# Kernel optimization log

Hardware: AMD Instinct MI355X
Metric: run time of the kernel (lower is better)

Reference implementation:

```python
import jax, jax.numpy as jnp
import numpy as np

B, S, D, H, HD, L, P = 32, 511, 512, 8, 64, 4, 501
PD = 32
FD = D - 2 * PD  # feature_proj output dim = hidden - 2*player_dim
DFF = 4 * D


def _pe(T, d):
    pos = jnp.arange(T, dtype=jnp.float32)[:, None]
    div = jnp.exp(jnp.arange(0, d, 2, dtype=jnp.float32) * (-np.log(10000.0) / d))
    pe = jnp.zeros((T, d), jnp.float32)
    pe = pe.at[:, 0::2].set(jnp.sin(pos * div))
    pe = pe.at[:, 1::2].set(jnp.cos(pos * div))
    return pe


def _ln(x, g, b, eps=1e-5):
    mu = x.mean(-1, keepdims=True)
    v = jnp.mean((x - mu) ** 2, -1, keepdims=True)
    return (x - mu) * jax.lax.rsqrt(v + eps) * g + b


def _forward(runs, wickets, overs, batters, bowlers, player_embed, Wf, bf,
             query_token, Wq, bq, Wk, bk, Wv, bv, Wo, bo,
             rec_s, bow_s, bat_s, W1, b1, W2, b2, g1, be1, g2, be2, Wout, bout):
    Bt, St = runs.shape
    T = St + 1
    # ball embedding: [B,S,3]@[3,FD] cat player embeds -> [B,S,D]
    feats = jnp.stack([runs, wickets, overs], -1) @ Wf + bf
    x = jnp.concatenate([feats, player_embed[batters], player_embed[bowlers]], -1)
    # append learned query token, add sinusoidal PE
    x = jnp.concatenate([x, jnp.broadcast_to(query_token, (Bt, 1, D))], 1)
    x = x + _pe(T, D)[None]
    # actor masks, padded with ones for the query row/col -> [B,T,T]
    sb = (bowlers[:, :, None] == bowlers[:, None, :]).astype(x.dtype)
    sm = (batters[:, :, None] == batters[:, None, :]).astype(x.dtype)
    row = jnp.ones((Bt, 1, St), x.dtype)
    col = jnp.ones((Bt, T, 1), x.dtype)
    sb = jnp.concatenate([jnp.concatenate([sb, row], 1), col], 2)
    sm = jnp.concatenate([jnp.concatenate([sm, row], 1), col], 2)
    causal = jnp.triu(jnp.ones((T, T), bool), 1)
    rec = jnp.arange(T, dtype=x.dtype) / T  # recency bias over key positions
    scale = 1.0 / np.float32(np.sqrt(HD))
    for l in range(L):
        q = (x @ Wq[l] + bq[l]).reshape(Bt, T, H, HD).transpose(0, 2, 1, 3)
        k = (x @ Wk[l] + bk[l]).reshape(Bt, T, H, HD).transpose(0, 2, 1, 3)
        v = (x @ Wv[l] + bv[l]).reshape(Bt, T, H, HD).transpose(0, 2, 1, 3)
        scores = jnp.einsum('bhqd,bhkd->bhqk', q, k) * scale
        # specialized head biases (num_heads >= 3)
        scores = scores.at[:, 0].add((rec_s[l] * rec)[None, None, :])
        scores = scores.at[:, 1].add(bow_s[l] * sb)
        scores = scores.at[:, 2].add(bat_s[l] * sm)
        scores = jnp.where(causal[None, None], -jnp.inf, scores)
        a = jax.nn.softmax(scores, axis=-1)
        o = jnp.einsum('bhqk,bhkd->bhqd', a, v).transpose(0, 2, 1, 3).reshape(Bt, T, D)
        x = _ln(x + o @ Wo[l] + bo[l], g1[l], be1[l])
        ff = jax.nn.gelu(x @ W1[l] + b1[l], approximate=False) @ W2[l] + b2[l]
        x = _ln(x + ff, g2[l], be2[l])
    return x[:, -1] @ Wout + bout  # [B, D]


def setup_inputs() -> dict:
    key = jax.random.key(0)
    ks = jax.random.split(key, 16)
    w = lambda k, sh: (0.02 * jax.random.normal(k, sh)).astype(jnp.float32)
    return {
        'runs': jax.random.uniform(ks[0], (B, S), jnp.float32),
        'wickets': jax.random.uniform(ks[1], (B, S), jnp.float32),
        'overs': jax.random.uniform(ks[2], (B, S), jnp.float32),
        'batters': jax.random.randint(ks[3], (B, S), 0, 500, jnp.int32),
        'bowlers': jax.random.randint(ks[4], (B, S), 0, 500, jnp.int32),
        'player_embed': w(ks[5], (P, PD)),
        'Wf': w(ks[6], (3, FD)), 'bf': jnp.zeros((FD,), jnp.float32),
        'query_token': jax.random.normal(ks[7], (1, 1, D), jnp.float32),
        'Wq': w(ks[8], (L, D, D)), 'bq': jnp.zeros((L, D), jnp.float32),
        'Wk': w(ks[9], (L, D, D)), 'bk': jnp.zeros((L, D), jnp.float32),
        'Wv': w(ks[10], (L, D, D)), 'bv': jnp.zeros((L, D), jnp.float32),
        'Wo': w(ks[11], (L, D, D)), 'bo': jnp.zeros((L, D), jnp.float32),
        'rec_s': jnp.full((L,), 0.5, jnp.float32),
        'bow_s': jnp.full((L,), 2.0, jnp.float32),
        'bat_s': jnp.full((L,), 2.0, jnp.float32),
        'W1': w(ks[12], (L, D, DFF)), 'b1': jnp.zeros((L, DFF), jnp.float32),
        'W2': w(ks[13], (L, DFF, D)), 'b2': jnp.zeros((L, D), jnp.float32),
        'g1': jnp.ones((L, D), jnp.float32), 'be1': jnp.zeros((L, D), jnp.float32),
        'g2': jnp.ones((L, D), jnp.float32), 'be2': jnp.zeros((L, D), jnp.float32),
        'Wout': w(ks[14], (D, D)), 'bout': jnp.zeros((D,), jnp.float32),
    }


def reference(runs, wickets, overs, batters, bowlers, player_embed, Wf, bf,
              query_token, Wq, bq, Wk, bk, Wv, bv, Wo, bo,
              rec_s, bow_s, bat_s, W1, b1, W2, b2, g1, be1, g2, be2, Wout, bout):
    return _forward(runs, wickets, overs, batters, bowlers, player_embed, Wf, bf,
                    query_token, Wq, bq, Wk, bk, Wv, bv, Wo, bo,
                    rec_s, bow_s, bat_s, W1, b1, W2, b2, g1, be1, g2, be2, Wout, bout)
```

## Files before the change

kernel.cpp:

```cpp
#include <hip/hip_runtime.h>
#include <math.h>

#define B_ 32
#define S_ 511
#define T_ 512
#define D_ 512
#define H_ 8
#define HD_ 64
#define L_ 4
#define P_ 501
#define PD_ 32
#define FD_ 448
#define DFF_ 2048

typedef __attribute__((ext_vector_type(8))) short bf16x8;
typedef __attribute__((ext_vector_type(4))) float f32x4;

__device__ __forceinline__ unsigned short f2bf(float f) {
  union { float f; unsigned int u; } c; c.f = f;
  unsigned int r = c.u + 0x7FFFu + ((c.u >> 16) & 1u);
  return (unsigned short)(r >> 16);
}

__global__ __launch_bounds__(256) void wtrans_kernel(
    const float* __restrict__ in, unsigned short* __restrict__ out, int K, int N)
{
  __shared__ float t[64][65];
  const int l = blockIdx.z;
  in  += (size_t)l * K * N;
  out += (size_t)l * N * K;
  const int k0 = blockIdx.x * 64, n0 = blockIdx.y * 64;
  const int tx = threadIdx.x & 63, ty = threadIdx.x >> 6;
#pragma unroll
  for (int i = 0; i < 16; ++i) {
    int r = ty + i * 4;
    t[r][tx] = in[(size_t)(k0 + r) * N + n0 + tx];
  }
  __syncthreads();
#pragma unroll
  for (int i = 0; i < 16; ++i) {
    int r = ty + i * 4;
    out[(size_t)(n0 + r) * K + k0 + tx] = f2bf(t[tx][r]);
  }
}

__global__ __launch_bounds__(256) void embed_kernel(
    const float* __restrict__ runs, const float* __restrict__ wickets,
    const float* __restrict__ overs, const int* __restrict__ batters,
    const int* __restrict__ bowlers, const float* __restrict__ pemb,
    const float* __restrict__ Wf, const float* __restrict__ bfv,
    const float* __restrict__ qtok, float* __restrict__ x,
    unsigned short* __restrict__ xb)
{
  size_t idx = (size_t)blockIdx.x * 256 + threadIdx.x;
  const size_t total = (size_t)B_ * T_ * D_;
  if (idx >= total) return;
  int d = (int)(idx % D_);
  int t = (int)((idx / D_) % T_);
  int b = (int)(idx / ((size_t)D_ * T_));
  float val;
  if (t < S_) {
    size_t st = (size_t)b * S_ + t;
    if (d < FD_) {
      val = runs[st] * Wf[d] + wickets[st] * Wf[FD_ + d] + overs[st] * Wf[2 * FD_ + d] + bfv[d];
    } else if (d < FD_ + PD_) {
      val = pemb[(size_t)batters[st] * PD_ + (d - FD_)];
    } else {
      val = pemb[(size_t)bowlers[st] * PD_ + (d - FD_ - PD_)];
    }
  } else {
    val = qtok[d];
  }
  float div = expf((float)(2 * (d >> 1)) * (-9.210340371976184f / (float)D_));
  float ang = (float)t * div;
  val += (d & 1) ? cosf(ang) : sinf(ang);
  x[idx] = val;
  xb[idx] = f2bf(val);
}

template<int ACT>
__global__ __launch_bounds__(256) void mfma_gemm(
    const unsigned short* __restrict__ A, const unsigned short* __restrict__ Bt,
    const float* __restrict__ bias, float* __restrict__ C,
    unsigned short* __restrict__ Cb, int N, int K)
{
  __shared__ unsigned short As[128 * 32];
  __shared__ unsigned short Bs[128 * 32];
  const int tid = threadIdx.x;
  const int m0 = blockIdx.y * 128, n0 = blockIdx.x * 128;
  const int lane = tid & 63, w = tid >> 6;
  const int wr = w >> 1, wc = w & 1;
  const int lr = lane & 15, lg = lane >> 4;

  f32x4 acc[4][4] = {};

  const int sr = tid >> 2, sc8 = (tid & 3) * 8;
  const unsigned short* gA = A + (size_t)(m0 + sr) * K + sc8;
  const unsigned short* gB = Bt + (size_t)(n0 + sr) * K + sc8;
  const size_t rowK64 = (size_t)64 * K;

  for (int k0 = 0; k0 < K; k0 += 32) {
    __syncthreads();
    *(bf16x8*)&As[sr * 32 + sc8]        = *(const bf16x8*)(gA + k0);
    *(bf16x8*)&As[(sr + 64) * 32 + sc8] = *(const bf16x8*)(gA + rowK64 + k0);
    *(bf16x8*)&Bs[sr * 32 + sc8]        = *(const bf16x8*)(gB + k0);
    *(bf16x8*)&Bs[(sr + 64) * 32 + sc8] = *(const bf16x8*)(gB + rowK64 + k0);
    __syncthreads();
    bf16x8 af[4], bfr[4];
#pragma unroll
    for (int f = 0; f < 4; ++f) {
      af[f]  = *(const bf16x8*)&As[(wr * 64 + f * 16 + lr) * 32 + lg * 8];
      bfr[f] = *(const bf16x8*)&Bs[(wc * 64 + f * 16 + lr) * 32 + lg * 8];
    }
#pragma unroll
    for (int i = 0; i < 4; ++i)
#pragma unroll
      for (int j = 0; j < 4; ++j)
        acc[i][j] = __builtin_amdgcn_mfma_f32_16x16x32_bf16(af[i], bfr[j], acc[i][j], 0, 0, 0);
  }

  const int crow0 = m0 + wr * 64 + lg * 4;
  const int ccol0 = n0 + wc * 64 + lr;
#pragma unroll
  for (int i = 0; i < 4; ++i) {
#pragma unroll
    for (int j = 0; j < 4; ++j) {
      const int col = ccol0 + j * 16;
      const float bcol = bias[col];
#pragma unroll
      for (int r = 0; r < 4; ++r) {
        const int row = crow0 + i * 16 + r;
        float v = acc[i][j][r] + bcol;
        if (ACT == 1) {
          v = 0.5f * v * (1.0f + erff(v * 0.70710678118654752f));
          Cb[(size_t)row * N + col] = f2bf(v);
        } else if (ACT == 2) {
          Cb[(size_t)row * N + col] = f2bf(v);
        } else {
          C[(size_t)row * N + col] = v;
        }
      }
    }
  }
}

__global__ __launch_bounds__(256) void vtrans_kernel(
    const unsigned short* __restrict__ vb, unsigned short* __restrict__ vt)
{
  __shared__ unsigned short tile[64 * 65];
  const int t0 = blockIdx.x * 64, h = blockIdx.y, b = blockIdx.z;
  const int tid = threadIdx.x;
  const int r = tid >> 2, ch = (tid & 3) * 16;
  const unsigned short* src = vb + ((size_t)b * T_ + t0 + r) * D_ + h * HD_ + ch;
  *(bf16x8*)&tile[r * 65 + ch]     = *(const bf16x8*)src;
  *(bf16x8*)&tile[r * 65 + ch + 8] = *(const bf16x8*)(src + 8);
  __syncthreads();
  unsigned short tmp[16];
#pragma unroll
  for (int j = 0; j < 16; ++j) tmp[j] = tile[(ch + j) * 65 + r];
  unsigned short* dst = vt + ((size_t)(b * H_ + h) * HD_ + r) * T_ + t0 + ch;
  *(bf16x8*)dst       = *(const bf16x8*)&tmp[0];
  *(bf16x8*)(dst + 8) = *(const bf16x8*)&tmp[8];
}

__global__ __launch_bounds__(256) void flash_mfma_kernel(
    const unsigned short* __restrict__ q, const unsigned short* __restrict__ k,
    const unsigned short* __restrict__ vt, unsigned short* __restrict__ o,
    const int* __restrict__ batters, const int* __restrict__ bowlers,
    const float* __restrict__ rec_sp, const float* __restrict__ bow_sp,
    const float* __restrict__ bat_sp, int l)
{
  __shared__ unsigned short QPs[64 * 70];
  __shared__ unsigned short Ks[64 * 70];
  __shared__ unsigned short Vs[64 * 70];
  __shared__ int aq_s[64], ak_s[64];

  const int qt = blockIdx.x, h = blockIdx.y, b = blockIdx.z;
  const int tid = threadIdx.x;
  const int w = tid >> 6, lane = tid & 63;
  const int c = lane & 15, g = lane >> 4;
  const int q0 = qt * 64;

  int mode = 0; float hs = 0.f;
  if (h == 0) { mode = 1; hs = rec_sp[l]; }
  else if (h == 1) { mode = 2; hs = bow_sp[l]; }
  else if (h == 2) { mode = 3; hs = bat_sp[l]; }
  const int* actors = (mode == 2) ? bowlers : batters;

  {
    const int r = tid >> 2, ch = (tid & 3) * 16;
    const unsigned short* src = q + ((size_t)b * T_ + q0 + r) * D_ + h * HD_ + ch;
    *(bf16x8*)&QPs[r * 70 + ch]     = *(const bf16x8*)src;
    *(bf16x8*)&QPs[r * 70 + ch + 8] = *(const bf16x8*)(src + 8);
  }
  if (tid < 64) {
    int qg_ = q0 + tid;
    aq_s[tid] = (mode >= 2 && qg_ < S_) ? actors[(size_t)b * S_ + qg_] : -1;
  }
  __syncthreads();

  bf16x8 af0 = *(const bf16x8*)&QPs[(w * 16 + c) * 70 + g * 8];
  bf16x8 af1 = *(const bf16x8*)&QPs[(w * 16 + c) * 70 + 32 + g * 8];

  int aq4[4];
#pragma unroll
  for (int r = 0; r < 4; ++r) aq4[r] = aq_s[w * 16 + 4 * g + r];

  float m_r[4] = {-INFINITY, -INFINITY, -INFINITY, -INFINITY};
  float l_r[4] = {0.f, 0.f, 0.f, 0.f};
  f32x4 o_acc[4] = {};

  for (int kt = 0; kt <= qt; ++kt) {
    const int k0 = kt * 64;
    __syncthreads();
    {
      const int r = tid >> 2, ch = (tid & 3) * 16;
      const unsigned short* ksrc = k + ((size_t)b * T_ + k0 + r) * D_ + h * HD_ + ch;
      *(bf16x8*)&Ks[r * 70 + ch]     = *(const bf16x8*)ksrc;
      *(bf16x8*)&Ks[r * 70 + ch + 8] = *(const bf16x8*)(ksrc + 8);
      const unsigned short* vsrc = vt + ((size_t)(b * H_ + h) * HD_ + r) * T_ + k0 + ch;
      *(bf16x8*)&Vs[r * 70 + ch]     = *(const bf16x8*)vsrc;
      *(bf16x8*)&Vs[r * 70 + ch + 8] = *(const bf16x8*)(vsrc + 8);
    }
    if (tid < 64) {
      int kg_ = k0 + tid;
      ak_s[tid] = (mode >= 2 && kg_ < S_) ? actors[(size_t)b * S_ + kg_] : -1;
    }
    __syncthreads();

    f32x4 s[4] = {};
#pragma unroll
    for (int f = 0; f < 4; ++f) {
      bf16x8 b0 = *(const bf16x8*)&Ks[(f * 16 + c) * 70 + g * 8];
      bf16x8 b1 = *(const bf16x8*)&Ks[(f * 16 + c) * 70 + 32 + g * 8];
      s[f] = __builtin_amdgcn_mfma_f32_16x16x32_bf16(af0, b0, s[f], 0, 0, 0);
      s[f] = __builtin_amdgcn_mfma_f32_16x16x32_bf16(af1, b1, s[f], 0, 0, 0);
    }

    int ak4[4];
#pragma unroll
    for (int f = 0; f < 4; ++f) ak4[f] = ak_s[f * 16 + c];
    float sv[4][4];
#pragma unroll
    for (int f = 0; f < 4; ++f) {
      const int kg = k0 + f * 16 + c;
#pragma unroll
      for (int r = 0; r < 4; ++r) {
        const int qg = q0 + w * 16 + 4 * g + r;
        float val = s[f][r] * 0.125f;
        if (mode == 1) {
          val = fmaf(hs, (float)kg * (1.0f / (float)T_), val);
        } else if (mode >= 2) {
          float eq = (qg == S_ || kg == S_) ? 1.0f : ((aq4[r] == ak4[f]) ? 1.0f : 0.0f);
          val = fmaf(hs, eq, val);
        }
        if (kg > qg) val = -INFINITY;
        sv[f][r] = val;
      }
    }

    float cr[4], rs[4];
#pragma unroll
    for (int r = 0; r < 4; ++r) {
      float pm = fmaxf(fmaxf(sv[0][r], sv[1][r]), fmaxf(sv[2][r], sv[3][r]));
      pm = fmaxf(pm, __shfl_xor(pm, 1));
      pm = fmaxf(pm, __shfl_xor(pm, 2));
      pm = fmaxf(pm, __shfl_xor(pm, 4));
      pm = fmaxf(pm, __shfl_xor(pm, 8));
      float m_new = fmaxf(m_r[r], pm);
      cr[r] = __expf(m_r[r] - m_new);
      m_r[r] = m_new;
      rs[r] = 0.f;
    }
#pragma unroll
    for (int f = 0; f < 4; ++f) {
#pragma unroll
      for (int r = 0; r < 4; ++r) {
        float p = __expf(sv[f][r] - m_r[r]);
        rs[r] += p;
        QPs[(w * 16 + 4 * g + r) * 70 + f * 16 + c] = f2bf(p);
      }
    }
#pragma unroll
    for (int r = 0; r < 4; ++r) {
      float t = rs[r];
      t += __shfl_xor(t, 1);
      t += __shfl_xor(t, 2);
      t += __shfl_xor(t, 4);
      t += __shfl_xor(t, 8);
      l_r[r] = l_r[r] * cr[r] + t;
#pragma unroll
      for (int f = 0; f < 4; ++f) o_acc[f][r] *= cr[r];
    }

    bf16x8 pa0 = *(const bf16x8*)&QPs[(w * 16 + c) * 70 + g * 8];
    bf16x8 pa1 = *(const bf16x8*)&QPs[(w * 16 + c) * 70 + 32 + g * 8];
#pragma unroll
    for (int f = 0; f < 4; ++f) {
      bf16x8 v0 = *(const bf16x8*)&Vs[(f * 16 + c) * 70 + g * 8];
      bf16x8 v1 = *(const bf16x8*)&Vs[(f * 16 + c) * 70 + 32 + g * 8];
      o_acc[f] = __builtin_amdgcn_mfma_f32_16x16x32_bf16(pa0, v0, o_acc[f], 0, 0, 0);
      o_acc[f] = __builtin_amdgcn_mfma_f32_16x16x32_bf16(pa1, v1, o_acc[f], 0, 0, 0);
    }
  }

  float inv[4];
#pragma unroll
  for (int r = 0; r < 4; ++r) inv[r] = 1.0f / l_r[r];
#pragma unroll
  for (int f = 0; f < 4; ++f) {
#pragma unroll
    for (int r = 0; r < 4; ++r) {
      const int row = q0 + w * 16 + 4 * g + r;
      o[((size_t)b * T_ + row) * D_ + h * HD_ + f * 16 + c] = f2bf(o_acc[f][r] * inv[r]);
    }
  }
}

__global__ __launch_bounds__(256) void add_ln_kernel(
    float* __restrict__ x, const float* __restrict__ y,
    const float* __restrict__ g, const float* __restrict__ be,
    unsigned short* __restrict__ xb)
{
  int row = blockIdx.x;
  int tid = threadIdx.x;
  size_t base = (size_t)row * D_;
  float v0 = x[base + tid] + y[base + tid];
  float v1 = x[base + tid + 256] + y[base + tid + 256];
  float s = v0 + v1;
  float s2 = v0 * v0 + v1 * v1;
  __shared__ float redA[4], redB[4];
#pragma unroll
  for (int off = 32; off > 0; off >>= 1) {
    s  += __shfl_down(s, off);
    s2 += __shfl_down(s2, off);
  }
  if ((tid & 63) == 0) { redA[tid >> 6] = s; redB[tid >> 6] = s2; }
  __syncthreads();
  float st  = redA[0] + redA[1] + redA[2] + redA[3];
  float s2t = redB[0] + redB[1] + redB[2] + redB[3];
  float mu = st * (1.0f / (float)D_);
  float var = s2t * (1.0f / (float)D_) - mu * mu;
  float r = rsqrtf(var + 1e-5f);
  float o0 = (v0 - mu) * r * g[tid] + be[tid];
  float o1 = (v1 - mu) * r * g[tid + 256] + be[tid + 256];
  x[base + tid]        = o0;
  x[base + tid + 256]  = o1;
  xb[base + tid]       = f2bf(o0);
  xb[base + tid + 256] = f2bf(o1);
}

__global__ __launch_bounds__(256) void final_kernel(
    const float* __restrict__ x, const float* __restrict__ Wout,
    const float* __restrict__ bout, float* __restrict__ out)
{
  __shared__ float xs[D_];
  int b = blockIdx.x;
  int n = blockIdx.y * 256 + threadIdx.x;
  const float* xr = x + ((size_t)b * T_ + (T_ - 1)) * D_;
  xs[threadIdx.x] = xr[threadIdx.x];
  xs[threadIdx.x + 256] = xr[threadIdx.x + 256];
  __syncthreads();
  float acc = bout[n];
  for (int kk = 0; kk < D_; ++kk)
    acc = fmaf(xs[kk], Wout[(size_t)kk * D_ + n], acc);
  out[(size_t)b * D_ + n] = acc;
}

extern "C" void kernel_launch(void* const* d_in, const int* in_sizes, int n_in,
                              void* d_out, int out_size, void* d_ws, size_t ws_size,
                              hipStream_t stream)
{
  const float* runs    = (const float*)d_in[0];
  const float* wickets = (const float*)d_in[1];
  const float* overs   = (const float*)d_in[2];
  const int*   batters = (const int*)d_in[3];
  const int*   bowlers = (const int*)d_in[4];
  const float* pemb    = (const float*)d_in[5];
  const float* Wf      = (const float*)d_in[6];
  const float* bfv     = (const float*)d_in[7];
  const float* qtok    = (const float*)d_in[8];
  const float* Wq      = (const float*)d_in[9];
  const float* bq      = (const float*)d_in[10];
  const float* Wk      = (const float*)d_in[11];
  const float* bk      = (const float*)d_in[12];
  const float* Wv      = (const float*)d_in[13];
  const float* bv      = (const float*)d_in[14];
  const float* Wo      = (const float*)d_in[15];
  const float* bo      = (const float*)d_in[16];
  const float* rec_s   = (const float*)d_in[17];
  const float* bow_s   = (const float*)d_in[18];
  const float* bat_s   = (const float*)d_in[19];
  const float* W1      = (const float*)d_in[20];
  const float* b1      = (const float*)d_in[21];
  const float* W2      = (const float*)d_in[22];
  const float* b2      = (const float*)d_in[23];
  const float* g1      = (const float*)d_in[24];
  const float* be1     = (const float*)d_in[25];
  const float* g2      = (const float*)d_in[26];
  const float* be2     = (const float*)d_in[27];
  const float* Wout    = (const float*)d_in[28];
  const float* bout    = (const float*)d_in[29];

  float* ws = (float*)d_ws;
  const size_t n1 = (size_t)B_ * T_ * D_;
  float* x  = ws;
  float* yb = ws + n1;
  unsigned short* xb   = (unsigned short*)(ws + 2 * n1);
  unsigned short* qb16 = xb + n1;
  unsigned short* kb16 = qb16 + n1;
  unsigned short* vb16 = kb16 + n1;
  unsigned short* vt   = vb16 + n1;
  unsigned short* ob   = vt + n1;
  unsigned short* wt   = ob + n1;
  unsigned short* hb   = qb16;

  const size_t wsz = (size_t)L_ * D_ * D_;
  unsigned short* wtq = wt;
  unsigned short* wtk = wtq + wsz;
  unsigned short* wtv = wtk + wsz;
  unsigned short* wto = wtv + wsz;
  unsigned short* wt1 = wto + wsz;
  unsigned short* wt2 = wt1 + (size_t)L_ * D_ * DFF_;

  const int M = B_ * T_;
  dim3 blk(256);

  wtrans_kernel<<<dim3(8, 8, L_),  blk, 0, stream>>>(Wq, wtq, D_, D_);
  wtrans_kernel<<<dim3(8, 8, L_),  blk, 0, stream>>>(Wk, wtk, D_, D_);
  wtrans_kernel<<<dim3(8, 8, L_),  blk, 0, stream>>>(Wv, wtv, D_, D_);
  wtrans_kernel<<<dim3(8, 8, L_),  blk, 0, stream>>>(Wo, wto, D_, D_);
  wtrans_kernel<<<dim3(8, 32, L_), blk, 0, stream>>>(W1, wt1, D_, DFF_);
  wtrans_kernel<<<dim3(32, 8, L_), blk, 0, stream>>>(W2, wt2, DFF_, D_);

  {
    size_t total = (size_t)B_ * T_ * D_;
    int nb = (int)((total + 255) / 256);
    embed_kernel<<<nb, blk, 0, stream>>>(runs, wickets, overs, batters, bowlers,
                                         pemb, Wf, bfv, qtok, x, xb);
  }

  for (int l = 0; l < L_; ++l) {
    mfma_gemm<2><<<dim3(D_ / 128, M / 128), blk, 0, stream>>>(
        xb, wtq + (size_t)l * D_ * D_, bq + l * D_, nullptr, qb16, D_, D_);
    mfma_gemm<2><<<dim3(D_ / 128, M / 128), blk, 0, stream>>>(
        xb, wtk + (size_t)l * D_ * D_, bk + l * D_, nullptr, kb16, D_, D_);
    mfma_gemm<2><<<dim3(D_ / 128, M / 128), blk, 0, stream>>>(
        xb, wtv + (size_t)l * D_ * D_, bv + l * D_, nullptr, vb16, D_, D_);

    vtrans_kernel<<<dim3(T_ / 64, H_, B_), blk, 0, stream>>>(vb16, vt);

    flash_mfma_kernel<<<dim3(T_ / 64, H_, B_), blk, 0, stream>>>(
        qb16, kb16, vt, ob, batters, bowlers, rec_s, bow_s, bat_s, l);

    mfma_gemm<0><<<dim3(D_ / 128, M / 128), blk, 0, stream>>>(
        ob, wto + (size_t)l * D_ * D_, bo + l * D_, yb, nullptr, D_, D_);
    add_ln_kernel<<<M, blk, 0, stream>>>(x, yb, g1 + l * D_, be1 + l * D_, xb);

    mfma_gemm<1><<<dim3(DFF_ / 128, M / 128), blk, 0, stream>>>(
        xb, wt1 + (size_t)l * D_ * DFF_, b1 + l * DFF_, nullptr, hb, DFF_, D_);
    mfma_gemm<0><<<dim3(D_ / 128, M / 128), blk, 0, stream>>>(
        hb, wt2 + (size_t)l * DFF_ * D_, b2 + l * D_, yb, nullptr, D_, DFF_);
    add_ln_kernel<<<M, blk, 0, stream>>>(x, yb, g2 + l * D_, be2 + l * D_, xb);
  }

  final_kernel<<<dim3(B_, D_ / 256), blk, 0, stream>>>(x, Wout, bout, (float*)d_out);
}
```

Baseline: 1.540 ms.

## Double-buffer GEMM via direct LDS loads, fuse V transpose, balance causal flash tiles

The GEMM now stages A/B tiles with global_load_lds into double-buffered shared memory, so the next K-slice is prefetched while MFMAs run on the current one. This also drops one barrier per iteration. A new ACT==3 epilogue writes V directly in head-transposed layout through a shared-memory tile, which removes the separate vtrans kernel. The flash kernel pairs query tile p with tile NT-1-p in each block to balance the causal work, and lets a wave skip key tiles that lie wholly above its rows. The trade-offs are more LDS per GEMM block and half as many flash blocks, which may lower occupancy.

```diff
diff --git a/kernel.cpp b/kernel.cpp
--- a/kernel.cpp
+++ b/kernel.cpp
@@ -15,6 +15,10 @@
 
 typedef __attribute__((ext_vector_type(8))) short bf16x8;
 typedef __attribute__((ext_vector_type(4))) float f32x4;
+
+#define GLDS16(gp, lp) __builtin_amdgcn_global_load_lds(                      \
+    (const __attribute__((address_space(1))) void*)(gp),                      \
+    (__attribute__((address_space(3))) void*)(lp), 16, 0, 0)
 
 __device__ __forceinline__ unsigned short f2bf(float f) {
   union { float f; unsigned int u; } c; c.f = f;
@@ -84,8 +88,9 @@
     const float* __restrict__ bias, float* __restrict__ C,
     unsigned short* __restrict__ Cb, int N, int K)
 {
-  __shared__ unsigned short As[128 * 32];
-  __shared__ unsigned short Bs[128 * 32];
+  __shared__ unsigned short As[2][128 * 32];
+  __shared__ unsigned short Bs[2][128 * 32];
+  __shared__ unsigned short Ts[ACT == 3 ? 128 * 136 : 1];
   const int tid = threadIdx.x;
   const int m0 = blockIdx.y * 128, n0 = blockIdx.x * 128;
   const int lane = tid & 63, w = tid >> 6;
@@ -94,30 +99,43 @@
 
   f32x4 acc[4][4] = {};
 
-  const int sr = tid >> 2, sc8 = (tid & 3) * 8;
-  const unsigned short* gA = A + (size_t)(m0 + sr) * K + sc8;
-  const unsigned short* gB = Bt + (size_t)(n0 + sr) * K + sc8;
-  const size_t rowK64 = (size_t)64 * K;
-
+  const int srow = w * 16 + (lane >> 2);
+  const int sc8 = (lane & 3) * 8;
+  const unsigned short* gA0 = A + (size_t)(m0 + srow) * K + sc8;
+  const unsigned short* gA1 = gA0 + (size_t)64 * K;
+  const unsigned short* gB0 = Bt + (size_t)(n0 + srow) * K + sc8;
+  const unsigned short* gB1 = gB0 + (size_t)64 * K;
+  const int lofs0 = (w * 16) * 32;
+  const int lofs1 = (64 + w * 16) * 32;
+
+#define STAGE(buf, kk)                                                        \
+  do {                                                                        \
+    GLDS16(gA0 + (kk), &As[buf][lofs0]);                                      \
+    GLDS16(gA1 + (kk), &As[buf][lofs1]);                                      \
+    GLDS16(gB0 + (kk), &Bs[buf][lofs0]);                                      \
+    GLDS16(gB1 + (kk), &Bs[buf][lofs1]);                                      \
+  } while (0)
+
+  STAGE(0, 0);
+  __syncthreads();
+  int cur = 0;
   for (int k0 = 0; k0 < K; k0 += 32) {
-    __syncthreads();
-    *(bf16x8*)&As[sr * 32 + sc8]        = *(const bf16x8*)(gA + k0);
-    *(bf16x8*)&As[(sr + 64) * 32 + sc8] = *(const bf16x8*)(gA + rowK64 + k0);
-    *(bf16x8*)&Bs[sr * 32 + sc8]        = *(const bf16x8*)(gB + k0);
-    *(bf16x8*)&Bs[(sr + 64) * 32 + sc8] = *(const bf16x8*)(gB + rowK64 + k0);
-    __syncthreads();
+    if (k0 + 32 < K) STAGE(cur ^ 1, k0 + 32);
     bf16x8 af[4], bfr[4];
 #pragma unroll
     for (int f = 0; f < 4; ++f) {
-      af[f]  = *(const bf16x8*)&As[(wr * 64 + f * 16 + lr) * 32 + lg * 8];
-      bfr[f] = *(const bf16x8*)&Bs[(wc * 64 + f * 16 + lr) * 32 + lg * 8];
+      af[f]  = *(const bf16x8*)&As[cur][(wr * 64 + f * 16 + lr) * 32 + lg * 8];
+      bfr[f] = *(const bf16x8*)&Bs[cur][(wc * 64 + f * 16 + lr) * 32 + lg * 8];
     }
 #pragma unroll
     for (int i = 0; i < 4; ++i)
 #pragma unroll
       for (int j = 0; j < 4; ++j)
         acc[i][j] = __builtin_amdgcn_mfma_f32_16x16x32_bf16(af[i], bfr[j], acc[i][j], 0, 0, 0);
-  }
+    __syncthreads();
+    cur ^= 1;
+  }
+#undef STAGE
 
   const int crow0 = m0 + wr * 64 + lg * 4;
   const int ccol0 = n0 + wc * 64 + lr;
@@ -136,31 +154,24 @@
           Cb[(size_t)row * N + col] = f2bf(v);
         } else if (ACT == 2) {
           Cb[(size_t)row * N + col] = f2bf(v);
+        } else if (ACT == 3) {
+          Ts[(wc * 64 + j * 16 + lr) * 136 + (wr * 64 + i * 16 + lg * 4 + r)] = f2bf(v);
         } else {
           C[(size_t)row * N + col] = v;
         }
       }
     }
   }
-}
-
-__global__ __launch_bounds__(256) void vtrans_kernel(
-    const unsigned short* __restrict__ vb, unsigned short* __restrict__ vt)
-{
-  __shared__ unsigned short tile[64 * 65];
-  const int t0 = blockIdx.x * 64, h = blockIdx.y, b = blockIdx.z;
-  const int tid = threadIdx.x;
-  const int r = tid >> 2, ch = (tid & 3) * 16;
-  const unsigned short* src = vb + ((size_t)b * T_ + t0 + r) * D_ + h * HD_ + ch;
-  *(bf16x8*)&tile[r * 65 + ch]     = *(const bf16x8*)src;
-  *(bf16x8*)&tile[r * 65 + ch + 8] = *(const bf16x8*)(src + 8);
-  __syncthreads();
-  unsigned short tmp[16];
-#pragma unroll
-  for (int j = 0; j < 16; ++j) tmp[j] = tile[(ch + j) * 65 + r];
-  unsigned short* dst = vt + ((size_t)(b * H_ + h) * HD_ + r) * T_ + t0 + ch;
-  *(bf16x8*)dst       = *(const bf16x8*)&tmp[0];
-  *(bf16x8*)(dst + 8) = *(const bf16x8*)&tmp[8];
+  if (ACT == 3) {
+    __syncthreads();
+    const int c = tid & 127, h2 = tid >> 7;
+    const int hh = (n0 + c) >> 6, hd = (n0 + c) & 63;
+    const int bb = m0 >> 9, t0 = (m0 & (T_ - 1)) + h2 * 64;
+    unsigned short* dst = Cb + (((size_t)bb * H_ + hh) * HD_ + hd) * T_ + t0;
+#pragma unroll
+    for (int e = 0; e < 8; ++e)
+      *(bf16x8*)(dst + e * 8) = *(const bf16x8*)&Ts[c * 136 + h2 * 64 + e * 8];
+  }
 }
 
 __global__ __launch_bounds__(256) void flash_mfma_kernel(
@@ -175,11 +186,11 @@
   __shared__ unsigned short Vs[64 * 70];
   __shared__ int aq_s[64], ak_s[64];
 
-  const int qt = blockIdx.x, h = blockIdx.y, b = blockIdx.z;
+  const int p = blockIdx.x, h = blockIdx.y, b = blockIdx.z;
   const int tid = threadIdx.x;
   const int w = tid >> 6, lane = tid & 63;
   const int c = lane & 15, g = lane >> 4;
-  const int q0 = qt * 64;
+  const int NT = T_ / 64;
 
   int mode = 0; float hs = 0.f;
   if (h == 0) { mode = 1; hs = rec_sp[l]; }
@@ -187,132 +198,136 @@
   else if (h == 2) { mode = 3; hs = bat_sp[l]; }
   const int* actors = (mode == 2) ? bowlers : batters;
 
-  {
-    const int r = tid >> 2, ch = (tid & 3) * 16;
-    const unsigned short* src = q + ((size_t)b * T_ + q0 + r) * D_ + h * HD_ + ch;
-    *(bf16x8*)&QPs[r * 70 + ch]     = *(const bf16x8*)src;
-    *(bf16x8*)&QPs[r * 70 + ch + 8] = *(const bf16x8*)(src + 8);
-  }
-  if (tid < 64) {
-    int qg_ = q0 + tid;
-    aq_s[tid] = (mode >= 2 && qg_ < S_) ? actors[(size_t)b * S_ + qg_] : -1;
-  }
-  __syncthreads();
-
-  bf16x8 af0 = *(const bf16x8*)&QPs[(w * 16 + c) * 70 + g * 8];
-  bf16x8 af1 = *(const bf16x8*)&QPs[(w * 16 + c) * 70 + 32 + g * 8];
-
-  int aq4[4];
-#pragma unroll
-  for (int r = 0; r < 4; ++r) aq4[r] = aq_s[w * 16 + 4 * g + r];
-
-  float m_r[4] = {-INFINITY, -INFINITY, -INFINITY, -INFINITY};
-  float l_r[4] = {0.f, 0.f, 0.f, 0.f};
-  f32x4 o_acc[4] = {};
-
-  for (int kt = 0; kt <= qt; ++kt) {
-    const int k0 = kt * 64;
+  const int sr = tid >> 2, sch = (tid & 3) * 16;
+
+  for (int ph = 0; ph < 2; ++ph) {
+    const int qt = (ph == 0) ? p : (NT - 1 - p);
+    const int q0 = qt * 64;
     __syncthreads();
+
     {
-      const int r = tid >> 2, ch = (tid & 3) * 16;
-      const unsigned short* ksrc = k + ((size_t)b * T_ + k0 + r) * D_ + h * HD_ + ch;
-      *(bf16x8*)&Ks[r * 70 + ch]     = *(const bf16x8*)ksrc;
-      *(bf16x8*)&Ks[r * 70 + ch + 8] = *(const bf16x8*)(ksrc + 8);
-      const unsigned short* vsrc = vt + ((size_t)(b * H_ + h) * HD_ + r) * T_ + k0 + ch;
-      *(bf16x8*)&Vs[r * 70 + ch]     = *(const bf16x8*)vsrc;
-      *(bf16x8*)&Vs[r * 70 + ch + 8] = *(const bf16x8*)(vsrc + 8);
+      const unsigned short* src = q + ((size_t)b * T_ + q0 + sr) * D_ + h * HD_ + sch;
+      *(bf16x8*)&QPs[sr * 70 + sch]     = *(const bf16x8*)src;
+      *(bf16x8*)&QPs[sr * 70 + sch + 8] = *(const bf16x8*)(src + 8);
     }
     if (tid < 64) {
-      int kg_ = k0 + tid;
-      ak_s[tid] = (mode >= 2 && kg_ < S_) ? actors[(size_t)b * S_ + kg_] : -1;
+      int qg_ = q0 + tid;
+      aq_s[tid] = (mode >= 2 && qg_ < S_) ? actors[(size_t)b * S_ + qg_] : -1;
     }
     __syncthreads();
 
-    f32x4 s[4] = {};
-#pragma unroll
-    for (int f = 0; f < 4; ++f) {
-      bf16x8 b0 = *(const bf16x8*)&Ks[(f * 16 + c) * 70 + g * 8];
-      bf16x8 b1 = *(const bf16x8*)&Ks[(f * 16 + c) * 70 + 32 + g * 8];
-      s[f] = __builtin_amdgcn_mfma_f32_16x16x32_bf16(af0, b0, s[f], 0, 0, 0);
-      s[f] = __builtin_amdgcn_mfma_f32_16x16x32_bf16(af1, b1, s[f], 0, 0, 0);
-    }
-
-    int ak4[4];
-#pragma unroll
-    for (int f = 0; f < 4; ++f) ak4[f] = ak_s[f * 16 + c];
-    float sv[4][4];
-#pragma unroll
-    for (int f = 0; f < 4; ++f) {
-      const int kg = k0 + f * 16 + c;
+    bf16x8 af0 = *(const bf16x8*)&QPs[(w * 16 + c) * 70 + g * 8];
+    bf16x8 af1 = *(const bf16x8*)&QPs[(w * 16 + c) * 70 + 32 + g * 8];
+    int aq4[4];
+#pragma unroll
+    for (int r = 0; r < 4; ++r) aq4[r] = aq_s[w * 16 + 4 * g + r];
+
+    float m_r[4] = {-INFINITY, -INFINITY, -INFINITY, -INFINITY};
+    float l_r[4] = {0.f, 0.f, 0.f, 0.f};
+    f32x4 o_acc[4] = {};
+
+    for (int kt = 0; kt <= qt; ++kt) {
+      const int k0 = kt * 64;
+      __syncthreads();
+      {
+        const unsigned short* ksrc = k + ((size_t)b * T_ + k0 + sr) * D_ + h * HD_ + sch;
+        *(bf16x8*)&Ks[sr * 70 + sch]     = *(const bf16x8*)ksrc;
+        *(bf16x8*)&Ks[sr * 70 + sch + 8] = *(const bf16x8*)(ksrc + 8);
+        const unsigned short* vsrc = vt + ((size_t)(b * H_ + h) * HD_ + sr) * T_ + k0 + sch;
+        *(bf16x8*)&Vs[sr * 70 + sch]     = *(const bf16x8*)vsrc;
+        *(bf16x8*)&Vs[sr * 70 + sch + 8] = *(const bf16x8*)(vsrc + 8);
+      }
+      if (tid < 64) {
+        int kg_ = k0 + tid;
+        ak_s[tid] = (mode >= 2 && kg_ < S_) ? actors[(size_t)b * S_ + kg_] : -1;
+      }
+      __syncthreads();
+
+      if (q0 + w * 16 + 15 < k0) continue;
+
+      f32x4 s[4] = {};
+#pragma unroll
+      for (int f = 0; f < 4; ++f) {
+        bf16x8 b0 = *(const bf16x8*)&Ks[(f * 16 + c) * 70 + g * 8];
+        bf16x8 b1 = *(const bf16x8*)&Ks[(f * 16 + c) * 70 + 32 + g * 8];
+        s[f] = __builtin_amdgcn_mfma_f32_16x16x32_bf16(af0, b0, s[f], 0, 0, 0);
+        s[f] = __builtin_amdgcn_mfma_f32_16x16x32_bf16(af1, b1, s[f], 0, 0, 0);
+      }
+
+      int ak4[4];
+#pragma unroll
+      for (int f = 0; f < 4; ++f) ak4[f] = ak_s[f * 16 + c];
+
+      float sv[4][4];
+#pragma unroll
+      for (int f = 0; f < 4; ++f) {
+        const int kg = k0 + f * 16 + c;
+#pragma unroll
+        for (int r = 0; r < 4; ++r) {
+          const int qg = q0 + w * 16 + 4 * g + r;
+          float val = s[f][r] * 0.125f;
+          if (mode == 1) {
+            val = fmaf(hs, (float)kg * (1.0f / (float)T_), val);
+          } else if (mode >= 2) {
+            float eq = (qg == S_ || kg == S_) ? 1.0f : ((aq4[r] == ak4[f]) ? 1.0f : 0.0f);
+            val = fmaf(hs, eq, val);
+          }
+          if (kg > qg) val = -INFINITY;
+          sv[f][r] = val;
+        }
+      }
+      float cr[4];
 #pragma unroll
       for (int r = 0; r < 4; ++r) {
-        const int qg = q0 + w * 16 + 4 * g + r;
-        float val = s[f][r] * 0.125f;
-        if (mode == 1) {
-          val = fmaf(hs, (float)kg * (1.0f / (float)T_), val);
-        } else if (mode >= 2) {
-          float eq = (qg == S_ || kg == S_) ? 1.0f : ((aq4[r] == ak4[f]) ? 1.0f : 0.0f);
-          val = fmaf(hs, eq, val);
+        float pm = fmaxf(fmaxf(sv[0][r], sv[1][r]), fmaxf(sv[2][r], sv[3][r]));
+        pm = fmaxf(pm, __shfl_xor(pm, 1));
+        pm = fmaxf(pm, __shfl_xor(pm, 2));
+        pm = fmaxf(pm, __shfl_xor(pm, 4));
+        pm = fmaxf(pm, __shfl_xor(pm, 8));
+        float m_new = fmaxf(m_r[r], pm);
+        cr[r] = __expf(m_r[r] - m_new);
+        m_r[r] = m_new;
+      }
+      float rs[4] = {0.f, 0.f, 0.f, 0.f};
+#pragma unroll
+      for (int f = 0; f < 4; ++f) {
+#pragma unroll
+        for (int r = 0; r < 4; ++r) {
+          float pv = __expf(sv[f][r] - m_r[r]);
+          rs[r] += pv;
+          QPs[(w * 16 + 4 * g + r) * 70 + f * 16 + c] = f2bf(pv);
         }
-        if (kg > qg) val = -INFINITY;
-        sv[f][r] = val;
-      }
-    }
-
-    float cr[4], rs[4];
+      }
+#pragma unroll
+      for (int r = 0; r < 4; ++r) {
+        float t = rs[r];
+        t += __shfl_xor(t, 1);
+        t += __shfl_xor(t, 2);
+        t += __shfl_xor(t, 4);
+        t += __shfl_xor(t, 8);
+        l_r[r] = l_r[r] * cr[r] + t;
+#pragma unroll
+        for (int f = 0; f < 4; ++f) o_acc[f][r] *= cr[r];
+      }
+
+      bf16x8 pa0 = *(const bf16x8*)&QPs[(w * 16 + c) * 70 + g * 8];
+      bf16x8 pa1 = *(const bf16x8*)&QPs[(w * 16 + c) * 70 + 32 + g * 8];
+#pragma unroll
+      for (int f = 0; f < 4; ++f) {
+        bf16x8 v0 = *(const bf16x8*)&Vs[(f * 16 + c) * 70 + g * 8];
+        bf16x8 v1 = *(const bf16x8*)&Vs[(f * 16 + c) * 70 + 32 + g * 8];
+        o_acc[f] = __builtin_amdgcn_mfma_f32_16x16x32_bf16(pa0, v0, o_acc[f], 0, 0, 0);
+        o_acc[f] = __builtin_amdgcn_mfma_f32_16x16x32_bf16(pa1, v1, o_acc[f], 0, 0, 0);
+      }
+    }
+
 #pragma unroll
     for (int r = 0; r < 4; ++r) {
-      float pm = fmaxf(fmaxf(sv[0][r], sv[1][r]), fmaxf(sv[2][r], sv[3][r]));
-      pm = fmaxf(pm, __shfl_xor(pm, 1));
-      pm = fmaxf(pm, __shfl_xor(pm, 2));
-      pm = fmaxf(pm, __shfl_xor(pm, 4));
-      pm = fmaxf(pm, __shfl_xor(pm, 8));
-      float m_new = fmaxf(m_r[r], pm);
-      cr[r] = __expf(m_r[r] - m_new);
-      m_r[r] = m_new;
-      rs[r] = 0.f;
-    }
-#pragma unroll
-    for (int f = 0; f < 4; ++f) {
-#pragma unroll
-      for (int r = 0; r < 4; ++r) {
-        float p = __expf(sv[f][r] - m_r[r]);
-        rs[r] += p;
-        QPs[(w * 16 + 4 * g + r) * 70 + f * 16 + c] = f2bf(p);
-      }
-    }
-#pragma unroll
-    for (int r = 0; r < 4; ++r) {
-      float t = rs[r];
-      t += __shfl_xor(t, 1);
-      t += __shfl_xor(t, 2);
-      t += __shfl_xor(t, 4);
-      t += __shfl_xor(t, 8);
-      l_r[r] = l_r[r] * cr[r] + t;
-#pragma unroll
-      for (int f = 0; f < 4; ++f) o_acc[f][r] *= cr[r];
-    }
-
-    bf16x8 pa0 = *(const bf16x8*)&QPs[(w * 16 + c) * 70 + g * 8];
-    bf16x8 pa1 = *(const bf16x8*)&QPs[(w * 16 + c) * 70 + 32 + g * 8];
-#pragma unroll
-    for (int f = 0; f < 4; ++f) {
-      bf16x8 v0 = *(const bf16x8*)&Vs[(f * 16 + c) * 70 + g * 8];
-      bf16x8 v1 = *(const bf16x8*)&Vs[(f * 16 + c) * 70 + 32 + g * 8];
-      o_acc[f] = __builtin_amdgcn_mfma_f32_16x16x32_bf16(pa0, v0, o_acc[f], 0, 0, 0);
-      o_acc[f] = __builtin_amdgcn_mfma_f32_16x16x32_bf16(pa1, v1, o_acc[f], 0, 0, 0);
-    }
-  }
-
-  float inv[4];
-#pragma unroll
-  for (int r = 0; r < 4; ++r) inv[r] = 1.0f / l_r[r];
-#pragma unroll
-  for (int f = 0; f < 4; ++f) {
-#pragma unroll
-    for (int r = 0; r < 4; ++r) {
+      const float inv = 1.0f / l_r[r];
       const int row = q0 + w * 16 + 4 * g + r;
-      o[((size_t)b * T_ + row) * D_ + h * HD_ + f * 16 + c] = f2bf(o_acc[f][r] * inv[r]);
+#pragma unroll
+      for (int f = 0; f < 4; ++f)
+        o[((size_t)b * T_ + row) * D_ + h * HD_ + f * 16 + c] = f2bf(o_acc[f][r] * inv);
     }
   }
 }
@@ -445,12 +460,10 @@
         xb, wtq + (size_t)l * D_ * D_, bq + l * D_, nullptr, qb16, D_, D_);
     mfma_gemm<2><<<dim3(D_ / 128, M / 128), blk, 0, stream>>>(
         xb, wtk + (size_t)l * D_ * D_, bk + l * D_, nullptr, kb16, D_, D_);
-    mfma_gemm<2><<<dim3(D_ / 128, M / 128), blk, 0, stream>>>(
-        xb, wtv + (size_t)l * D_ * D_, bv + l * D_, nullptr, vb16, D_, D_);
-
-    vtrans_kernel<<<dim3(T_ / 64, H_, B_), blk, 0, stream>>>(vb16, vt);
-
-    flash_mfma_kernel<<<dim3(T_ / 64, H_, B_), blk, 0, stream>>>(
+    mfma_gemm<3><<<dim3(D_ / 128, M / 128), blk, 0, stream>>>(
+        xb, wtv + (size_t)l * D_ * D_, bv + l * D_, nullptr, vt, D_, D_);
+
+    flash_mfma_kernel<<<dim3(T_ / 128, H_, B_), blk, 0, stream>>>(
         qb16, kb16, vt, ob, batters, bowlers, rec_s, bow_s, bat_s, l);
 
     mfma_gemm<0><<<dim3(D_ / 128, M / 128), blk, 0, stream>>>(
```

Measured after the change: 1.399 ms. 1.1x faster.
